# Performance work log

Measured on AMD Instinct MI355X. Metric: run time of the kernel, lower is better.

## Reference

```python
import math
import jax, jax.numpy as jnp
import numpy as np

NEG_INF = -jnp.inf


def setup_inputs() -> dict:
    key = jax.random.key(0)
    k1, k2, k3 = jax.random.split(key, 3)
    B, T, D = 2, 2048, 1024
    x = jax.random.normal(k1, (B, T, D), dtype=jnp.float32)
    w_qkv = jax.random.normal(k2, (3 * D, D), dtype=jnp.float32) * (1.0 / math.sqrt(D))
    w_out = jax.random.normal(k3, (D, D), dtype=jnp.float32) * (1.0 / math.sqrt(D))
    return {"x": x, "w_qkv": w_qkv, "w_out": w_out, "n_heads": 16, "k": 8}


def reference(x, w_qkv, w_out, n_heads, k):
    B, T, D = x.shape
    head_dim = D // n_heads
    scale = math.sqrt(head_dim)

    qkv = x @ w_qkv.T                                   # (B,T,3D), torch Linear: x W^T
    q, kk, v = jnp.split(qkv, 3, axis=-1)

    def split_heads(t):
        return t.reshape(B, T, n_heads, head_dim).transpose(0, 2, 1, 3)  # (B,H,T,dh)

    q, kk, v = split_heads(q), split_heads(kk), split_heads(v)

    scores = jnp.einsum("bhqd,bhkd->bhqk", q, kk) / scale  # (B,H,T,T)
    causal = jnp.tril(jnp.ones((T, T), dtype=bool))
    scores = jnp.where(causal, scores, NEG_INF)

    # per-row effective k: min(k, n_valid) with n_valid = row index + 1
    top_vals = jax.lax.top_k(scores, k)[0]                 # (B,H,T,k), sorted desc
    k_eff_idx = jnp.minimum(jnp.arange(1, T + 1), k) - 1   # (T,)
    thresh = jnp.take_along_axis(
        top_vals, k_eff_idx[None, None, :, None], axis=-1  # (B,H,T,1)
    )
    keep = scores >= thresh                                # ties kept, matching torch >=
    scores = jnp.where(keep, scores, NEG_INF)

    attn = jax.nn.softmax(scores, axis=-1)
    attn = jnp.nan_to_num(attn)                            # defensive; rows never all -inf
    out = jnp.einsum("bhqk,bhkd->bhqd", attn, v)
    out = out.transpose(0, 2, 1, 3).reshape(B, T, D)       # merge heads
    return out @ w_out.T
```

## Files before the change

kernel.cpp:

```cpp
#include <hip/hip_runtime.h>
#include <hip/hip_bf16.h>
#include <math.h>
#include <float.h>

#define NUM_B 2
#define SEQ_T 2048
#define DIM_D 1024
#define NH 16
#define DH 64
#define KDIM 1024
#define KSEL 8

#define CAP 32
#define MFMA_MARGIN 0.06f

typedef __attribute__((ext_vector_type(8))) short bf16x8v;
typedef __attribute__((ext_vector_type(4))) float f32x4v;
typedef __attribute__((ext_vector_type(4))) double f64x4v;

__device__ __forceinline__ float bf2f(unsigned int u) {
  union { unsigned int i; float f; } v; v.i = u << 16; return v.f;
}

__device__ __forceinline__ short f2bs(float f) {
  __hip_bfloat16 h = __float2bfloat16(f);
  return *(short*)&h;
}

__device__ __forceinline__ void split8(float4 x0, float4 x1,
                                       unsigned short* __restrict__ hp,
                                       unsigned short* __restrict__ lp) {
  unsigned short h[8], l[8];
  const float xs[8] = {x0.x, x0.y, x0.z, x0.w, x1.x, x1.y, x1.z, x1.w};
#pragma unroll
  for (int j = 0; j < 8; ++j) {
    const short hb = f2bs(xs[j]);
    h[j] = (unsigned short)hb;
    const float hf = bf2f((unsigned int)(unsigned short)hb);
    l[j] = (unsigned short)f2bs(xs[j] - hf);
  }
  *(uint4*)hp = *(const uint4*)h;
  *(uint4*)lp = *(const uint4*)l;
}

__global__ __launch_bounds__(512) void gemm_qk(
    const float* __restrict__ A, const float* __restrict__ Bm,
    float* __restrict__ qbuf, float* __restrict__ kbuf,
    unsigned short* __restrict__ kbf) {
  __shared__ __align__(16) float As[64][36];
  __shared__ __align__(16) float Bs[128][36];
  const int tid = threadIdx.x;
  const int lane = tid & 63;
  const int w = tid >> 6;
  const int row0 = blockIdx.y * 64;
  const int col0 = blockIdx.x * 128;
  const int lrA = tid >> 3;
  const int lkA = (tid & 7) << 2;
  const int lrB = tid >> 2;
  const int lkB = (tid & 3) << 3;
  const float* ap = A + (size_t)(row0 + lrA) * KDIM + lkA;
  const float* bp = Bm + (size_t)(col0 + lrB) * KDIM + lkB;
  const int wr = (w >> 2) << 5;
  const int wc = (w & 3) << 5;
  const int li = lane & 15;
  const int lk4 = lane >> 4;

  int rowof[4], colof[4];
  {
    f64x4v pr = {0.0, 0.0, 0.0, 0.0};
    f64x4v pc = {0.0, 0.0, 0.0, 0.0};
    const double vidx = (double)li;
    pr = __builtin_amdgcn_mfma_f64_16x16x4f64(vidx, 1.0, pr, 0, 0, 0);
    pc = __builtin_amdgcn_mfma_f64_16x16x4f64(1.0, vidx, pc, 0, 0, 0);
#pragma unroll
    for (int vj = 0; vj < 4; ++vj) {
      rowof[vj] = (int)(pr[vj] * 0.25 + 0.5);
      colof[vj] = (int)(pc[vj] * 0.25 + 0.5);
    }
  }

  f64x4v acc[2][2];
#pragma unroll
  for (int m = 0; m < 2; ++m)
#pragma unroll
    for (int n = 0; n < 2; ++n)
      acc[m][n] = (f64x4v){0.0, 0.0, 0.0, 0.0};

  float4 ra = *(const float4*)(ap);
  float4 rb0 = *(const float4*)(bp);
  float4 rb1 = *(const float4*)(bp + 4);
  for (int k0 = 0; k0 < KDIM; k0 += 32) {
    __syncthreads();
    *(float4*)&As[lrA][lkA] = ra;
    *(float4*)&Bs[lrB][lkB] = rb0;
    *(float4*)&Bs[lrB][lkB + 4] = rb1;
    if (k0 + 32 < KDIM) {
      ra = *(const float4*)(ap + k0 + 32);
      rb0 = *(const float4*)(bp + k0 + 32);
      rb1 = *(const float4*)(bp + k0 + 36);
    }
    __syncthreads();
#pragma unroll
    for (int ks = 0; ks < 32; ks += 4) {
      const int kk = ks + lk4;
      const double af0 = (double)As[wr + li][kk];
      const double af1 = (double)As[wr + 16 + li][kk];
      const double bf0 = (double)Bs[wc + li][kk];
      const double bf1 = (double)Bs[wc + 16 + li][kk];
      acc[0][0] = __builtin_amdgcn_mfma_f64_16x16x4f64(af0, bf0, acc[0][0], 0, 0, 0);
      acc[0][1] = __builtin_amdgcn_mfma_f64_16x16x4f64(af0, bf1, acc[0][1], 0, 0, 0);
      acc[1][0] = __builtin_amdgcn_mfma_f64_16x16x4f64(af1, bf0, acc[1][0], 0, 0, 0);
      acc[1][1] = __builtin_amdgcn_mfma_f64_16x16x4f64(af1, bf1, acc[1][1], 0, 0, 0);
    }
  }

  const int bb = row0 >> 11;
  const int t0 = row0 & 2047;
#pragma unroll
  for (int m = 0; m < 2; ++m)
#pragma unroll
    for (int n = 0; n < 2; ++n)
#pragma unroll
      for (int vj = 0; vj < 4; ++vj) {
        const int r = wr + 16 * m + rowof[vj];
        const int gc = col0 + wc + 16 * n + colof[vj];
        const int qi = gc >> 10;
        const int head = (gc & 1023) >> 6;
        const int d = gc & 63;
        const int t = t0 + r;
        const float fv = (float)acc[m][n][vj];
        float* dst = ((qi == 0) ? qbuf : kbuf) +
                     (size_t)(bb * NH + head) * SEQ_T * DH;
        dst[(size_t)t * DH + d] = fv;
        if (qi == 1) {
          unsigned short* kb = kbf + ((size_t)(bb * NH + head) << 17);
          const int key = t & 127;
          const int off =
              (((t >> 7) << 13) | (key << 6) | d) ^ ((key & 7) << 3);
          __hip_bfloat16 hb = __float2bfloat16(fv);
          kb[off] = *(unsigned short*)&hb;
        }
      }
}

__global__ __launch_bounds__(256) void gemm_v(
    const float* __restrict__ A, const float* __restrict__ Bm,
    unsigned short* __restrict__ vbuf) {
  __shared__ __align__(16) unsigned short Ah[64][40];
  __shared__ __align__(16) unsigned short Al[64][40];
  __shared__ __align__(16) unsigned short Bh[64][40];
  __shared__ __align__(16) unsigned short Bl[64][40];
  const int tid = threadIdx.x;
  const int lane = tid & 63;
  const int w = tid >> 6;
  const int row0 = blockIdx.y * 64;
  const int col0 = blockIdx.x * 64;
  const int lrow = tid >> 2;
  const int lk = (tid & 3) << 3;
  const float* ap = A + (size_t)(row0 + lrow) * KDIM + lk;
  const float* bp = Bm + (size_t)(col0 + lrow) * KDIM + lk;
  const int wr = (w >> 1) << 5;
  const int wc = (w & 1) << 5;
  const int li = lane & 15;
  const int kA = (lane >> 4) << 3;

  f32x4v acc[2][2];
#pragma unroll
  for (int m = 0; m < 2; ++m)
#pragma unroll
    for (int n = 0; n < 2; ++n)
      acc[m][n] = (f32x4v){0.f, 0.f, 0.f, 0.f};

  float4 ra0 = *(const float4*)(ap);
  float4 ra1 = *(const float4*)(ap + 4);
  float4 rb0 = *(const float4*)(bp);
  float4 rb1 = *(const float4*)(bp + 4);
  for (int k0 = 0; k0 < KDIM; k0 += 32) {
    __syncthreads();
    split8(ra0, ra1, &Ah[lrow][lk], &Al[lrow][lk]);
    split8(rb0, rb1, &Bh[lrow][lk], &Bl[lrow][lk]);
    if (k0 + 32 < KDIM) {
      ra0 = *(const float4*)(ap + k0 + 32);
      ra1 = *(const float4*)(ap + k0 + 36);
      rb0 = *(const float4*)(bp + k0 + 32);
      rb1 = *(const float4*)(bp + k0 + 36);
    }
    __syncthreads();
    bf16x8v ah[2], al[2], bh[2], bl[2];
#pragma unroll
    for (int m = 0; m < 2; ++m) {
      ah[m] = *(const bf16x8v*)&Ah[wr + 16 * m + li][kA];
      al[m] = *(const bf16x8v*)&Al[wr + 16 * m + li][kA];
      bh[m] = *(const bf16x8v*)&Bh[wc + 16 * m + li][kA];
      bl[m] = *(const bf16x8v*)&Bl[wc + 16 * m + li][kA];
    }
#pragma unroll
    for (int m = 0; m < 2; ++m)
#pragma unroll
      for (int n = 0; n < 2; ++n) {
        acc[m][n] = __builtin_amdgcn_mfma_f32_16x16x32_bf16(ah[m], bh[n], acc[m][n], 0, 0, 0);
        acc[m][n] = __builtin_amdgcn_mfma_f32_16x16x32_bf16(ah[m], bl[n], acc[m][n], 0, 0, 0);
        acc[m][n] = __builtin_amdgcn_mfma_f32_16x16x32_bf16(al[m], bh[n], acc[m][n], 0, 0, 0);
      }
  }

  const int head = col0 >> 6;
  const int bb = row0 >> 11;
  const int t0 = row0 & 2047;
  unsigned short* dst = vbuf + (size_t)(bb * NH + head) * SEQ_T * DH;
  const int r4 = (lane >> 4) << 2;
#pragma unroll
  for (int m = 0; m < 2; ++m)
#pragma unroll
    for (int n = 0; n < 2; ++n)
#pragma unroll
      for (int j = 0; j < 4; ++j) {
        const int t = t0 + wr + 16 * m + r4 + j;
        const int d = wc + 16 * n + li;
        dst[(size_t)t * DH + d] = (unsigned short)f2bs(acc[m][n][j]);
      }
}

__global__ __launch_bounds__(256) void attn_topk(
    const float* __restrict__ q, const float* __restrict__ kmat,
    const unsigned short* __restrict__ kbf,
    const unsigned short* __restrict__ v, unsigned short* __restrict__ ctx) {
  __shared__ __align__(16) unsigned short kt[128 * 64];
  __shared__ double cs64[64][CAP];
  __shared__ short ckey[64][CAP];
  __shared__ int ccnt[64];
  __shared__ double rthr[64];
  __shared__ float rmx[64];

  const int tid = threadIdx.x;
  const int lane = tid & 63;
  const int w = tid >> 6;
  const int bh = blockIdx.x & 31;
  const int t0 = (blockIdx.x >> 5) << 6;
  const size_t kbase = (size_t)bh * SEQ_T * DH;
  const int wrow0 = t0 + (w << 4);
  const int kA = (lane >> 4) << 3;
  const int rbase = wrow0 + ((lane >> 4) << 2);

  bf16x8v qa0, qa1;
  {
    const float* qr = q + kbase + (size_t)(wrow0 + (lane & 15)) * DH;
    const float4 x0 = *(const float4*)(qr + kA);
    const float4 x1 = *(const float4*)(qr + kA + 4);
    const float4 y0 = *(const float4*)(qr + 32 + kA);
    const float4 y1 = *(const float4*)(qr + 32 + kA + 4);
    qa0[0] = f2bs(x0.x); qa0[1] = f2bs(x0.y);
    qa0[2] = f2bs(x0.z); qa0[3] = f2bs(x0.w);
    qa0[4] = f2bs(x1.x); qa0[5] = f2bs(x1.y);
    qa0[6] = f2bs(x1.z); qa0[7] = f2bs(x1.w);
    qa1[0] = f2bs(y0.x); qa1[1] = f2bs(y0.y);
    qa1[2] = f2bs(y0.z); qa1[3] = f2bs(y0.w);
    qa1[4] = f2bs(y1.x); qa1[5] = f2bs(y1.y);
    qa1[6] = f2bs(y1.z); qa1[7] = f2bs(y1.w);
  }

  const uint4* ksrc = (const uint4*)(kbf + ((size_t)bh << 17));
  const int nt = (t0 >> 7) + 1;
  const int wmax = wrow0 + 15;

  float tq[4][8];
#pragma unroll
  for (int j = 0; j < 4; ++j)
#pragma unroll
    for (int m = 0; m < 8; ++m) tq[j][m] = -FLT_MAX;

  for (int T = 0; T < nt; ++T) {
    if (T) __syncthreads();
    {
      const uint4* st = ksrc + (size_t)T * 1024;
      uint4* dv = (uint4*)kt;
#pragma unroll
      for (int i = 0; i < 4; ++i) dv[i * 256 + tid] = st[i * 256 + tid];
    }
    __syncthreads();
    const int glim0 = (wmax - (T << 7)) >> 4;
    const int glim = glim0 > 7 ? 7 : glim0;
    for (int gt = 0; gt <= glim; ++gt) {
      const int kk = (gt << 4) + (lane & 15);
      const int key = (T << 7) + kk;
      const int b0 = ((kk << 7) | (kA << 1)) ^ ((kk & 7) << 4);
      const int b1 = ((kk << 7) | ((32 + kA) << 1)) ^ ((kk & 7) << 4);
      const bf16x8v kb0 = *(const bf16x8v*)((const char*)kt + b0);
      const bf16x8v kb1 = *(const bf16x8v*)((const char*)kt + b1);
      f32x4v acc = {0.f, 0.f, 0.f, 0.f};
      acc = __builtin_amdgcn_mfma_f32_16x16x32_bf16(qa0, kb0, acc, 0, 0, 0);
      acc = __builtin_amdgcn_mfma_f32_16x16x32_bf16(qa1, kb1, acc, 0, 0, 0);
#pragma unroll
      for (int j = 0; j < 4; ++j) {
        float sc = acc[j] * 0.125f;
        sc = (key <= rbase + j) ? sc : -FLT_MAX;
        if (sc > tq[j][7]) {
          float s = sc;
#pragma unroll
          for (int m = 0; m < 8; ++m) {
            const float hi = fmaxf(tq[j][m], s);
            s = fminf(tq[j][m], s);
            tq[j][m] = hi;
          }
        }
      }
    }
  }

#pragma unroll
  for (int j = 0; j < 4; ++j) {
#pragma unroll
    for (int xm = 1; xm < 16; xm <<= 1) {
      float m[8];
#pragma unroll
      for (int i = 0; i < 8; ++i) {
        const float pb = __shfl_xor(tq[j][7 - i], xm);
        m[i] = fmaxf(tq[j][i], pb);
      }
#pragma unroll
      for (int d = 4; d >= 1; d >>= 1)
#pragma unroll
        for (int i = 0; i < 8; ++i)
          if ((i & d) == 0 && (i | d) < 8) {
            const float hi = fmaxf(m[i], m[i | d]);
            const float lo = fminf(m[i], m[i | d]);
            m[i] = hi;
            m[i | d] = lo;
          }
#pragma unroll
      for (int i = 0; i < 8; ++i) tq[j][i] = m[i];
    }
  }
  float thrj[4];
#pragma unroll
  for (int j = 0; j < 4; ++j) {
    const int kf = (rbase + j + 1 < KSEL) ? (rbase + j + 1) : KSEL;
    float th = tq[j][7];
#pragma unroll
    for (int m = 0; m < 8; ++m)
      if (m == kf - 1) th = tq[j][m];
    thrj[j] = th - MFMA_MARGIN;
  }

  if (tid < 64) ccnt[tid] = 0;
  __syncthreads();

  for (int T = 0; T < nt; ++T) {
    if (T) __syncthreads();
    {
      const uint4* st = ksrc + (size_t)T * 1024;
      uint4* dv = (uint4*)kt;
#pragma unroll
      for (int i = 0; i < 4; ++i) dv[i * 256 + tid] = st[i * 256 + tid];
    }
    __syncthreads();
    const int glim0 = (wmax - (T << 7)) >> 4;
    const int glim = glim0 > 7 ? 7 : glim0;
    for (int gt = 0; gt <= glim; ++gt) {
      const int kk = (gt << 4) + (lane & 15);
      const int key = (T << 7) + kk;
      const int b0 = ((kk << 7) | (kA << 1)) ^ ((kk & 7) << 4);
      const int b1 = ((kk << 7) | ((32 + kA) << 1)) ^ ((kk & 7) << 4);
      const bf16x8v kb0 = *(const bf16x8v*)((const char*)kt + b0);
      const bf16x8v kb1 = *(const bf16x8v*)((const char*)kt + b1);
      f32x4v acc = {0.f, 0.f, 0.f, 0.f};
      acc = __builtin_amdgcn_mfma_f32_16x16x32_bf16(qa0, kb0, acc, 0, 0, 0);
      acc = __builtin_amdgcn_mfma_f32_16x16x32_bf16(qa1, kb1, acc, 0, 0, 0);
#pragma unroll
      for (int j = 0; j < 4; ++j) {
        const float sc = acc[j] * 0.125f;
        if (key <= rbase + j && sc >= thrj[j]) {
          const int rl = (w << 4) + ((lane >> 4) << 2) + j;
          const int p = atomicAdd(&ccnt[rl], 1);
          if (p < CAP) ckey[rl][p] = (short)key;
        }
      }
    }
  }

  const int lid = lane & 31;
  for (int rp = 0; rp < 8; ++rp) {
    const int rl = (w << 4) + (rp << 1) + (lane >> 5);
    const int ncc = ccnt[rl] < CAP ? ccnt[rl] : CAP;
    if (lid < ncc) {
      const int key = ckey[rl][lid];
      const float* qr = q + kbase + (size_t)(t0 + rl) * DH;
      const float* kr = kmat + kbase + (size_t)key * DH;
      double s = 0.0;
#pragma unroll
      for (int d4 = 0; d4 < 16; ++d4) {
        const float4 qq = *(const float4*)(qr + (d4 << 2));
        const float4 kq = *(const float4*)(kr + (d4 << 2));
        s = fma((double)qq.x, (double)kq.x, s);
        s = fma((double)qq.y, (double)kq.y, s);
        s = fma((double)qq.z, (double)kq.z, s);
        s = fma((double)qq.w, (double)kq.w, s);
      }
      cs64[rl][lid] = s * 0.125;
    }
  }
  __syncthreads();

  if (lane < 16) {
    const int rl = (w << 4) + lane;
    const int trow = t0 + rl;
    const int ncc = ccnt[rl] < CAP ? ccnt[rl] : CAP;
    double a64[8];
#pragma unroll
    for (int j = 0; j < 8; ++j) a64[j] = -DBL_MAX;
    for (int l = 0; l < ncc; ++l) {
      double sv = cs64[rl][l];
#pragma unroll
      for (int j = 0; j < 8; ++j) {
        const double hi = fmax(a64[j], sv);
        sv = fmin(a64[j], sv);
        a64[j] = hi;
      }
    }
    const int kf = (trow + 1 < KSEL) ? (trow + 1) : KSEL;
    double th = a64[7];
#pragma unroll
    for (int j = 0; j < 8; ++j)
      if (j == kf - 1) th = a64[j];
    rthr[rl] = th;
    rmx[rl] = (float)a64[0];
  }
  __syncthreads();

  for (int rg = 0; rg < 4; ++rg) {
    const int rlb = (w << 4) + (rg << 2);
    float acv[4] = {0.f, 0.f, 0.f, 0.f};
    float Zs[4] = {0.f, 0.f, 0.f, 0.f};
    int ncs[4];
    double ths[4];
    float mxs[4];
#pragma unroll
    for (int j = 0; j < 4; ++j) {
      const int rl = rlb + j;
      ncs[j] = ccnt[rl] < CAP ? ccnt[rl] : CAP;
      ths[j] = rthr[rl];
      mxs[j] = rmx[rl];
    }
    int nmax = ncs[0];
#pragma unroll
    for (int j = 1; j < 4; ++j) nmax = ncs[j] > nmax ? ncs[j] : nmax;
    for (int l = 0; l < nmax; ++l) {
#pragma unroll
      for (int j = 0; j < 4; ++j) {
        const int rl = rlb + j;
        if (l < ncs[j]) {
          const double s = cs64[rl][l];
          const float wgl = (s >= ths[j]) ? expf((float)s - mxs[j]) : 0.f;
          Zs[j] += wgl;
          acv[j] = fmaf(
              wgl,
              bf2f((unsigned int)v[kbase + (size_t)ckey[rl][l] * DH + lane]),
              acv[j]);
        }
      }
    }
#pragma unroll
    for (int j = 0; j < 4; ++j) {
      const int trow = t0 + rlb + j;
      __hip_bfloat16 h = __float2bfloat16(acv[j] / Zs[j]);
      ctx[((size_t)(bh >> 4) * SEQ_T + trow) * DIM_D + (bh & 15) * DH + lane] =
          *(unsigned short*)&h;
    }
  }
}

__global__ __launch_bounds__(256) void gemm_out(
    const unsigned short* __restrict__ A, const float* __restrict__ Bm,
    float* __restrict__ obuf) {
  __shared__ __align__(16) unsigned short Ah[64][40];
  __shared__ __align__(16) unsigned short Bh[64][40];
  __shared__ __align__(16) unsigned short Bl[64][40];
  const int tid = threadIdx.x;
  const int lane = tid & 63;
  const int w = tid >> 6;
  const int row0 = blockIdx.y * 64;
  const int col0 = blockIdx.x * 64;
  const int lrow = tid >> 2;
  const int lk = (tid & 3) << 3;
  const unsigned short* ap = A + (size_t)(row0 + lrow) * KDIM + lk;
  const float* bp = Bm + (size_t)(col0 + lrow) * KDIM + lk;
  const int wr = (w >> 1) << 5;
  const int wc = (w & 1) << 5;
  const int li = lane & 15;
  const int kA = (lane >> 4) << 3;

  f32x4v acc[2][2];
#pragma unroll
  for (int m = 0; m < 2; ++m)
#pragma unroll
    for (int n = 0; n < 2; ++n)
      acc[m][n] = (f32x4v){0.f, 0.f, 0.f, 0.f};

  uint4 ua = *(const uint4*)(ap);
  float4 rb0 = *(const float4*)(bp);
  float4 rb1 = *(const float4*)(bp + 4);
  for (int k0 = 0; k0 < KDIM; k0 += 32) {
    __syncthreads();
    *(uint4*)&Ah[lrow][lk] = ua;
    split8(rb0, rb1, &Bh[lrow][lk], &Bl[lrow][lk]);
    if (k0 + 32 < KDIM) {
      ua = *(const uint4*)(ap + k0 + 32);
      rb0 = *(const float4*)(bp + k0 + 32);
      rb1 = *(const float4*)(bp + k0 + 36);
    }
    __syncthreads();
    bf16x8v ah[2], bh[2], bl[2];
#pragma unroll
    for (int m = 0; m < 2; ++m) {
      ah[m] = *(const bf16x8v*)&Ah[wr + 16 * m + li][kA];
      bh[m] = *(const bf16x8v*)&Bh[wc + 16 * m + li][kA];
      bl[m] = *(const bf16x8v*)&Bl[wc + 16 * m + li][kA];
    }
#pragma unroll
    for (int m = 0; m < 2; ++m)
#pragma unroll
      for (int n = 0; n < 2; ++n) {
        acc[m][n] = __builtin_amdgcn_mfma_f32_16x16x32_bf16(ah[m], bh[n], acc[m][n], 0, 0, 0);
        acc[m][n] = __builtin_amdgcn_mfma_f32_16x16x32_bf16(ah[m], bl[n], acc[m][n], 0, 0, 0);
      }
  }

  const int r4 = (lane >> 4) << 2;
#pragma unroll
  for (int m = 0; m < 2; ++m)
#pragma unroll
    for (int n = 0; n < 2; ++n)
#pragma unroll
      for (int j = 0; j < 4; ++j) {
        const int r = row0 + wr + 16 * m + r4 + j;
        const int c = col0 + wc + 16 * n + li;
        obuf[(size_t)r * DIM_D + c] = acc[m][n][j];
      }
}

extern "C" void kernel_launch(void* const* d_in, const int* in_sizes, int n_in,
                              void* d_out, int out_size, void* d_ws,
                              size_t ws_size, hipStream_t stream) {
  (void)out_size; (void)ws_size;
  const float* x = (const float*)d_in[0];
  const float* wqkv = (const float*)d_in[1];
  const float* wout = (const float*)d_in[2];
  for (int i = 0; i < n_in; ++i) {
    if (in_sizes[i] == NUM_B * SEQ_T * DIM_D) x = (const float*)d_in[i];
    else if (in_sizes[i] == 3 * DIM_D * DIM_D) wqkv = (const float*)d_in[i];
    else if (in_sizes[i] == DIM_D * DIM_D) wout = (const float*)d_in[i];
  }
  float* out = (float*)d_out;

  const size_t qkv_elems = (size_t)NUM_B * NH * SEQ_T * DH;
  float* qbuf = (float*)d_ws;
  float* kbuf = qbuf + qkv_elems;
  unsigned short* vbuf = (unsigned short*)(kbuf + qkv_elems);
  unsigned short* ctxb = vbuf + qkv_elems;
  unsigned short* kbf = ctxb + (size_t)NUM_B * SEQ_T * DIM_D;

  gemm_qk<<<dim3(2 * DIM_D / 128, NUM_B * SEQ_T / 64), 512, 0, stream>>>(
      x, wqkv, qbuf, kbuf, kbf);
  gemm_v<<<dim3(DIM_D / 64, NUM_B * SEQ_T / 64), 256, 0, stream>>>(
      x, wqkv + (size_t)2 * DIM_D * KDIM, vbuf);
  attn_topk<<<dim3(NUM_B * NH * (SEQ_T / 64)), 256, 0, stream>>>(
      qbuf, kbuf, kbf, vbuf, ctxb);
  gemm_out<<<dim3(DIM_D / 64, NUM_B * SEQ_T / 64), 256, 0, stream>>>(
      ctxb, wout, out);
}
```

Measured before the change: 609.6 us.

## Widen V GEMM tile to 64x128 and permute attention tile scheduling order

The V projection GEMM now uses 512-thread blocks covering 128 output columns (two heads) instead of 64. Each A tile is loaded and split into bf16 hi/lo parts once per two heads, which halves A re-reads and the grid size. The causal attention kernel also remaps blockIdx to query-tile order so that heavy late tiles and light early tiles are interleaved, aiming to balance load across CUs. The wider tile uses more LDS and registers per block, which may lower occupancy.

Measured after the change: 592.4 us. 1.03x faster.

```diff
diff --git a/kernel.cpp b/kernel.cpp
--- a/kernel.cpp
+++ b/kernel.cpp
@@ -41,6 +41,22 @@
   }
   *(uint4*)hp = *(const uint4*)h;
   *(uint4*)lp = *(const uint4*)l;
+}
+
+__device__ __forceinline__ void split4(float4 x,
+                                       unsigned short* __restrict__ hp,
+                                       unsigned short* __restrict__ lp) {
+  unsigned short h[4], l[4];
+  const float xs[4] = {x.x, x.y, x.z, x.w};
+#pragma unroll
+  for (int j = 0; j < 4; ++j) {
+    const short hb = f2bs(xs[j]);
+    h[j] = (unsigned short)hb;
+    const float hf = bf2f((unsigned int)(unsigned short)hb);
+    l[j] = (unsigned short)f2bs(xs[j] - hf);
+  }
+  *(uint2*)hp = *(const uint2*)h;
+  *(uint2*)lp = *(const uint2*)l;
 }
 
 __global__ __launch_bounds__(512) void gemm_qk(
@@ -143,24 +159,26 @@
       }
 }
 
-__global__ __launch_bounds__(256) void gemm_v(
+__global__ __launch_bounds__(512) void gemm_v(
     const float* __restrict__ A, const float* __restrict__ Bm,
     unsigned short* __restrict__ vbuf) {
   __shared__ __align__(16) unsigned short Ah[64][40];
   __shared__ __align__(16) unsigned short Al[64][40];
-  __shared__ __align__(16) unsigned short Bh[64][40];
-  __shared__ __align__(16) unsigned short Bl[64][40];
+  __shared__ __align__(16) unsigned short Bh[128][40];
+  __shared__ __align__(16) unsigned short Bl[128][40];
   const int tid = threadIdx.x;
   const int lane = tid & 63;
   const int w = tid >> 6;
   const int row0 = blockIdx.y * 64;
-  const int col0 = blockIdx.x * 64;
-  const int lrow = tid >> 2;
-  const int lk = (tid & 3) << 3;
-  const float* ap = A + (size_t)(row0 + lrow) * KDIM + lk;
-  const float* bp = Bm + (size_t)(col0 + lrow) * KDIM + lk;
-  const int wr = (w >> 1) << 5;
-  const int wc = (w & 1) << 5;
+  const int col0v = blockIdx.x * 128;
+  const int lrA = tid >> 3;
+  const int lkA = (tid & 7) << 2;
+  const int lrB = tid >> 2;
+  const int lkB = (tid & 3) << 3;
+  const float* ap = A + (size_t)(row0 + lrA) * KDIM + lkA;
+  const float* bp = Bm + (size_t)(col0v + lrB) * KDIM + lkB;
+  const int wr = (w >> 2) << 5;
+  const int wc = (w & 3) << 5;
   const int li = lane & 15;
   const int kA = (lane >> 4) << 3;
 
@@ -171,17 +189,15 @@
     for (int n = 0; n < 2; ++n)
       acc[m][n] = (f32x4v){0.f, 0.f, 0.f, 0.f};
 
-  float4 ra0 = *(const float4*)(ap);
-  float4 ra1 = *(const float4*)(ap + 4);
+  float4 ra = *(const float4*)(ap);
   float4 rb0 = *(const float4*)(bp);
   float4 rb1 = *(const float4*)(bp + 4);
   for (int k0 = 0; k0 < KDIM; k0 += 32) {
     __syncthreads();
-    split8(ra0, ra1, &Ah[lrow][lk], &Al[lrow][lk]);
-    split8(rb0, rb1, &Bh[lrow][lk], &Bl[lrow][lk]);
+    split4(ra, &Ah[lrA][lkA], &Al[lrA][lkA]);
+    split8(rb0, rb1, &Bh[lrB][lkB], &Bl[lrB][lkB]);
     if (k0 + 32 < KDIM) {
-      ra0 = *(const float4*)(ap + k0 + 32);
-      ra1 = *(const float4*)(ap + k0 + 36);
+      ra = *(const float4*)(ap + k0 + 32);
       rb0 = *(const float4*)(bp + k0 + 32);
       rb1 = *(const float4*)(bp + k0 + 36);
     }
@@ -204,10 +220,8 @@
       }
   }
 
-  const int head = col0 >> 6;
   const int bb = row0 >> 11;
   const int t0 = row0 & 2047;
-  unsigned short* dst = vbuf + (size_t)(bb * NH + head) * SEQ_T * DH;
   const int r4 = (lane >> 4) << 2;
 #pragma unroll
   for (int m = 0; m < 2; ++m)
@@ -216,8 +230,11 @@
 #pragma unroll
       for (int j = 0; j < 4; ++j) {
         const int t = t0 + wr + 16 * m + r4 + j;
-        const int d = wc + 16 * n + li;
-        dst[(size_t)t * DH + d] = (unsigned short)f2bs(acc[m][n][j]);
+        const int vcol = col0v + wc + 16 * n + li;
+        const int head = vcol >> 6;
+        const int d = vcol & 63;
+        vbuf[(size_t)(bb * NH + head) * SEQ_T * DH + (size_t)t * DH + d] =
+            (unsigned short)f2bs(acc[m][n][j]);
       }
 }
 
@@ -236,7 +253,13 @@
   const int lane = tid & 63;
   const int w = tid >> 6;
   const int bh = blockIdx.x & 31;
-  const int t0 = (blockIdx.x >> 5) << 6;
+  const int u = blockIdx.x >> 5;
+  int g;
+  if (u < 8) g = u;
+  else if (u < 16) g = 23 - u;
+  else if (u < 24) g = u;
+  else g = 55 - u;
+  const int t0 = g << 6;
   const size_t kbase = (size_t)bh * SEQ_T * DH;
   const int wrow0 = t0 + (w << 4);
   const int kA = (lane >> 4) << 3;
@@ -561,7 +584,7 @@
 
   gemm_qk<<<dim3(2 * DIM_D / 128, NUM_B * SEQ_T / 64), 512, 0, stream>>>(
       x, wqkv, qbuf, kbuf, kbf);
-  gemm_v<<<dim3(DIM_D / 64, NUM_B * SEQ_T / 64), 256, 0, stream>>>(
+  gemm_v<<<dim3(DIM_D / 128, NUM_B * SEQ_T / 64), 512, 0, stream>>>(
       x, wqkv + (size_t)2 * DIM_D * KDIM, vbuf);
   attn_topk<<<dim3(NUM_B * NH * (SEQ_T / 64)), 256, 0, stream>>>(
       qbuf, kbuf, kbf, vbuf, ctxb);
```
